# Kernel optimization log

Measured on AMD Instinct MI355X. Metric: run time of the kernel, lower is better.

## Reference

```python
import jax, jax.numpy as jnp
import numpy as np

HIDDEN = 2048
N_HEADS = 16
HEAD_DIM = HIDDEN // N_HEADS
INV_NORM = 1.0 / float(np.sqrt(HEAD_DIM))
BETA = 1.0


def setup_inputs() -> dict:
    key = jax.random.key(0)
    ks = jax.random.split(key, 12)
    B, S, H = 2, 2048, HIDDEN
    scale = 1.0 / float(np.sqrt(H))
    return {
        "hidden_states": jax.random.normal(ks[0], (B, S, H), jnp.float32),
        "residual": jax.random.normal(ks[1], (B, S, H), jnp.float32),
        "alibi": jax.random.normal(ks[2], (B * N_HEADS, 1, S), jnp.float32),
        "Wq": jax.random.normal(ks[3], (H, H), jnp.float32) * scale,
        "bq": jnp.zeros((H,), jnp.float32),
        "Wk": jax.random.normal(ks[4], (H, H), jnp.float32) * scale,
        "bk": jnp.zeros((H,), jnp.float32),
        "Wv": jax.random.normal(ks[5], (H, H), jnp.float32) * scale,
        "bv": jnp.zeros((H,), jnp.float32),
        "Wd": jax.random.normal(ks[6], (H, H), jnp.float32) * scale,
        "bd": jnp.zeros((H,), jnp.float32),
    }


def reference(hidden_states, residual, alibi, Wq, bq, Wk, bk, Wv, bv, Wd, bd):
    B, S, H = hidden_states.shape
    # separate QKV projections (nn.Linear: x @ W^T + b)
    q = hidden_states @ Wq.T + bq
    k = hidden_states @ Wk.T + bk
    v = hidden_states @ Wv.T + bv
    # [B, n_heads, S, head_dim]
    q = q.reshape(B, S, N_HEADS, HEAD_DIM).transpose(0, 2, 1, 3)
    k = k.reshape(B, S, N_HEADS, HEAD_DIM).transpose(0, 2, 1, 3)
    v = v.reshape(B, S, N_HEADS, HEAD_DIM).transpose(0, 2, 1, 3)
    # baddbmm: scores = beta * alibi + inv_norm * q @ k^T, per (batch*head)
    alibi_bh = alibi.reshape(B, N_HEADS, 1, S)  # broadcasts over query dim
    scores = BETA * alibi_bh + INV_NORM * jnp.einsum("bhqd,bhkd->bhqk", q, k)
    probs = jax.nn.softmax(scores.astype(jnp.float32), axis=-1).astype(v.dtype)
    # attention dropout: p=0.0 (identity)
    ctx = jnp.einsum("bhqk,bhkd->bhqd", probs, v)  # [B,H,S,D]
    ctx = ctx.transpose(0, 2, 1, 3).reshape(B, S, H)
    out = ctx @ Wd.T + bd
    # hidden dropout p=0.0 then residual add (dropout_add)
    return out + residual
```

## Files before the change

kernel.cpp:

```cpp
#include <hip/hip_runtime.h>

#define HID   2048
#define NHEAD 16
#define HD    128
#define SEQ   2048
#define BATCH 2
#define MROWS (BATCH*SEQ)
#define NQKV  (3*HID)
#define INV_NORM 0.08838834764831845f
#define LOG2E    1.4426950408889634f
#define SCALE_L2 (INV_NORM*LOG2E)

typedef __attribute__((ext_vector_type(8)))  __bf16 bf16x8;
typedef __attribute__((ext_vector_type(4)))  float  f32x4;
typedef __attribute__((ext_vector_type(16))) float  f32x16;

typedef __attribute__((address_space(1))) void GV;
typedef __attribute__((address_space(3))) void LV;

__device__ __forceinline__ void async16(const void* g, void* l) {
  __builtin_amdgcn_global_load_lds((const GV*)g, (LV*)l, 16, 0, 0);
}

__device__ __forceinline__ unsigned short f2bf(float f) {
  unsigned u = __builtin_bit_cast(unsigned, f);
  u += 0x7FFFu + ((u >> 16) & 1u);
  return (unsigned short)(u >> 16);
}

__device__ __forceinline__ unsigned pkbf(float a, float b) {
#if __has_builtin(__builtin_amdgcn_cvt_pk_bf16_f32)
  typedef __attribute__((ext_vector_type(2))) __bf16 bf16x2;
  bf16x2 r = __builtin_amdgcn_cvt_pk_bf16_f32(a, b);
  return __builtin_bit_cast(unsigned, r);
#else
  return (unsigned)f2bf(a) | ((unsigned)f2bf(b) << 16);
#endif
}

__device__ __forceinline__ void mfma16(f32x4& c, bf16x8 a, bf16x8 b) {
  c = __builtin_amdgcn_mfma_f32_16x16x32_bf16(a, b, c, 0, 0, 0);
}

__device__ __forceinline__ bf16x8 frag(const unsigned short* buf, int row, int chunk) {
  return *(const bf16x8*)(buf + ((row * 8 + (chunk ^ (row & 7))) << 3));
}

__global__ __launch_bounds__(256) void cvt_kernel(const float* __restrict__ src,
                                                  unsigned short* __restrict__ dst, int n) {
  int i = (blockIdx.x * 256 + threadIdx.x) * 4;
  if (i >= n) return;
  float4 v = *(const float4*)(src + i);
  ushort4 o;
  o.x = f2bf(v.x); o.y = f2bf(v.y); o.z = f2bf(v.z); o.w = f2bf(v.w);
  *(ushort4*)(dst + i) = o;
}

__global__ __launch_bounds__(256) void cvtw_kernel(const float* __restrict__ W0,
                                                   const float* __restrict__ W1,
                                                   const float* __restrict__ W2,
                                                   const float* __restrict__ W3,
                                                   unsigned short* __restrict__ dst) {
  int sel = blockIdx.y;
  const float* src = (sel == 0) ? W0 : (sel == 1) ? W1 : (sel == 2) ? W2 : W3;
  unsigned short* d = dst + (size_t)sel * HID * HID;
  int i = (blockIdx.x * 256 + threadIdx.x) * 4;
  float4 v = *(const float4*)(src + i);
  ushort4 o;
  o.x = f2bf(v.x); o.y = f2bf(v.y); o.z = f2bf(v.z); o.w = f2bf(v.w);
  *(ushort4*)(d + i) = o;
}

__device__ __forceinline__ void gemm_core(const unsigned short* __restrict__ A,
                                          const unsigned short* __restrict__ Bm,
                                          int K, int m0, int n0,
                                          unsigned short* As, unsigned short* Bs,
                                          f32x4 (&acc)[4][4]) {
  const int tid  = threadIdx.x;
  const int w    = tid >> 6;
  const int lane = tid & 63;
  const int l16  = lane & 15;
  const int quad = lane >> 4;
  const int wm   = (w & 1) * 64;
  const int wn   = (w >> 1) * 64;

  const f32x4 zero = {0.f, 0.f, 0.f, 0.f};
#pragma unroll
  for (int i = 0; i < 4; ++i)
#pragma unroll
    for (int j = 0; j < 4; ++j) acc[i][j] = zero;

  for (int k0 = 0; k0 < K; k0 += 64) {
    __syncthreads();
#pragma unroll
    for (int i = 0; i < 4; ++i) {
      int slot = i * 256 + w * 64 + lane;
      int r = slot >> 3;
      int c = (slot & 7) ^ (r & 7);
      async16(A  + (size_t)(m0 + r) * K + k0 + c * 8, (char*)As + (size_t)(i * 256 + w * 64) * 16);
      async16(Bm + (size_t)(n0 + r) * K + k0 + c * 8, (char*)Bs + (size_t)(i * 256 + w * 64) * 16);
    }
    __syncthreads();

#pragma unroll
    for (int kk = 0; kk < 2; ++kk) {
      bf16x8 af[4], bfp[4];
#pragma unroll
      for (int i = 0; i < 4; ++i) af[i]  = frag(As, wm + i * 16 + l16, kk * 4 + quad);
#pragma unroll
      for (int j = 0; j < 4; ++j) bfp[j] = frag(Bs, wn + j * 16 + l16, kk * 4 + quad);
#pragma unroll
      for (int i = 0; i < 4; ++i)
#pragma unroll
        for (int j = 0; j < 4; ++j) mfma16(acc[i][j], af[i], bfp[j]);
    }
  }
}

#define ASZ (256 * 64)

__global__ __launch_bounds__(512, 2) void gemm_qkv256_kernel(
    const unsigned short* __restrict__ Xb, const unsigned short* __restrict__ Wb,
    const float* __restrict__ bq, const float* __restrict__ bk,
    const float* __restrict__ bv, unsigned short* __restrict__ Cout) {
  __shared__ __align__(16) unsigned short As[2 * ASZ];
  __shared__ __align__(16) unsigned short Bs[2 * ASZ];

  const int tid  = threadIdx.x;
  const int w    = tid >> 6;
  const int lane = tid & 63;
  const int l16  = lane & 15;
  const int quad = lane >> 4;
  const int wm   = (w & 1) * 128;
  const int wn   = (w >> 1) * 64;

  const int wg = blockIdx.x;
  const int sw = (wg & 7) * 48 + (wg >> 3);
  const int m0 = (sw & 15) * 256;
  const int n0 = (sw >> 4) * 256;

  const unsigned short* Ag = Xb + (size_t)m0 * HID;
  const unsigned short* Bg = Wb + (size_t)n0 * HID;

  const int sr  = tid >> 3;
  const int scs = ((tid & 7) ^ (sr & 7)) * 8;

#define STG(SRC, DST, RB, KO)                                        \
  async16((SRC) + (size_t)((RB) + sr) * HID + (KO) + scs,            \
          (char*)(DST) + (((RB) * 8 + w * 64) * 16))

  f32x4 acc[8][4];
  const f32x4 zero = {0.f, 0.f, 0.f, 0.f};
#pragma unroll
  for (int a = 0; a < 8; ++a)
#pragma unroll
    for (int j = 0; j < 4; ++j) acc[a][j] = zero;

  STG(Ag, As, 0, 0);  STG(Ag, As, 64, 0);  STG(Ag, As, 128, 0);  STG(Ag, As, 192, 0);
  STG(Bg, Bs, 0, 0);  STG(Bg, Bs, 64, 0);  STG(Bg, Bs, 128, 0);  STG(Bg, Bs, 192, 0);
  STG(Ag, As + ASZ, 0, 64);  STG(Ag, As + ASZ, 128, 64);
  asm volatile("s_waitcnt vmcnt(2)" ::: "memory");
  __builtin_amdgcn_s_barrier();

  for (int i = 0; i < 16; ++i) {
    const int k1 = (2 * i + 1) * 64;
    const int t2 = 2 * i + 2, t3 = 2 * i + 3;
    const int k2 = (t2 < 32 ? t2 : 31) * 64;
    const int k3 = (t3 < 32 ? t3 : 31) * 64;
    bf16x8 tb0[4], tb1[4];

    {
      bf16x8 ta[4];
#pragma unroll
      for (int ii = 0; ii < 4; ++ii) ta[ii] = frag(As, wm + ii * 16 + l16, quad);
#pragma unroll
      for (int j = 0; j < 4; ++j) tb0[j] = frag(Bs, wn + j * 16 + l16, quad);
      STG(Ag, As + ASZ, 64, k1);
      STG(Ag, As + ASZ, 192, k1);
      __builtin_amdgcn_s_barrier();
      asm volatile("s_waitcnt lgkmcnt(0)" ::: "memory");
      __builtin_amdgcn_s_setprio(1);
#pragma unroll
      for (int ii = 0; ii < 4; ++ii)
#pragma unroll
        for (int j = 0; j < 4; ++j) mfma16(acc[ii][j], ta[ii], tb0[j]);
      __builtin_amdgcn_s_setprio(0);
      __builtin_amdgcn_s_barrier();
    }
    {
      bf16x8 ta[4];
#pragma unroll
      for (int ii = 0; ii < 4; ++ii) ta[ii] = frag(As, wm + ii * 16 + l16, 4 + quad);
#pragma unroll
      for (int j = 0; j < 4; ++j) tb1[j] = frag(Bs, wn + j * 16 + l16, 4 + quad);
      STG(Bg, Bs + ASZ, 0, k1);
      STG(Bg, Bs + ASZ, 64, k1);
      __builtin_amdgcn_s_barrier();
      asm volatile("s_waitcnt lgkmcnt(0)" ::: "memory");
      __builtin_amdgcn_s_setprio(1);
#pragma unroll
      for (int ii = 0; ii < 4; ++ii)
#pragma unroll
        for (int j = 0; j < 4; ++j) mfma16(acc[ii][j], ta[ii], tb1[j]);
      __builtin_amdgcn_s_setprio(0);
      __builtin_amdgcn_s_barrier();
    }
    {
      bf16x8 ta[4];
#pragma unroll
      for (int ii = 0; ii < 4; ++ii) ta[ii] = frag(As, wm + 64 + ii * 16 + l16, quad);
      STG(Bg, Bs + ASZ, 128, k1);
      STG(Bg, Bs + ASZ, 192, k1);
      __builtin_amdgcn_s_barrier();
      asm volatile("s_waitcnt lgkmcnt(0)" ::: "memory");
      __builtin_amdgcn_s_setprio(1);
#pragma unroll
      for (int ii = 0; ii < 4; ++ii)
#pragma unroll
        for (int j = 0; j < 4; ++j) mfma16(acc[4 + ii][j], ta[ii], tb0[j]);
      __builtin_amdgcn_s_setprio(0);
      __builtin_amdgcn_s_barrier();
    }
    {
      bf16x8 ta[4];
#pragma unroll
      for (int ii = 0; ii < 4; ++ii) ta[ii] = frag(As, wm + 64 + ii * 16 + l16, 4 + quad);
      STG(Ag, As, 0, k2);
      STG(Ag, As, 128, k2);
      __builtin_amdgcn_s_barrier();
      asm volatile("s_waitcnt lgkmcnt(0)" ::: "memory");
      __builtin_amdgcn_s_setprio(1);
#pragma unroll
      for (int ii = 0; ii < 4; ++ii)
#pragma unroll
        for (int j = 0; j < 4; ++j) mfma16(acc[4 + ii][j], ta[ii], tb1[j]);
      __builtin_amdgcn_s_setprio(0);
      asm volatile("s_waitcnt vmcnt(2)" ::: "memory");
      __builtin_amdgcn_s_barrier();
    }
    {
      bf16x8 ta[4];
#pragma unroll
      for (int ii = 0; ii < 4; ++ii) ta[ii] = frag(As + ASZ, wm + ii * 16 + l16, quad);
#pragma unroll
      for (int j = 0; j < 4; ++j) tb0[j] = frag(Bs + ASZ, wn + j * 16 + l16, quad);
      STG(Ag, As, 64, k2);
      STG(Ag, As, 192, k2);
      __builtin_amdgcn_s_barrier();
      asm volatile("s_waitcnt lgkmcnt(0)" ::: "memory");
      __builtin_amdgcn_s_setprio(1);
#pragma unroll
      for (int ii = 0; ii < 4; ++ii)
#pragma unroll
        for (int j = 0; j < 4; ++j) mfma16(acc[ii][j], ta[ii], tb0[j]);
      __builtin_amdgcn_s_setprio(0);
      __builtin_amdgcn_s_barrier();
    }
    {
      bf16x8 ta[4];
#pragma unroll
      for (int ii = 0; ii < 4; ++ii) ta[ii] = frag(As + ASZ, wm + ii * 16 + l16, 4 + quad);
#pragma unroll
      for (int j = 0; j < 4; ++j) tb1[j] = frag(Bs + ASZ, wn + j * 16 + l16, 4 + quad);
      STG(Bg, Bs, 0, k2);
      STG(Bg, Bs, 64, k2);
      __builtin_amdgcn_s_barrier();
      asm volatile("s_waitcnt lgkmcnt(0)" ::: "memory");
      __builtin_amdgcn_s_setprio(1);
#pragma unroll
      for (int ii = 0; ii < 4; ++ii)
#pragma unroll
        for (int j = 0; j < 4; ++j) mfma16(acc[ii][j], ta[ii], tb1[j]);
      __builtin_amdgcn_s_setprio(0);
      __builtin_amdgcn_s_barrier();
    }
    {
      bf16x8 ta[4];
#pragma unroll
      for (int ii = 0; ii < 4; ++ii) ta[ii] = frag(As + ASZ, wm + 64 + ii * 16 + l16, quad);
      STG(Bg, Bs, 128, k2);
      STG(Bg, Bs, 192, k2);
      __builtin_amdgcn_s_barrier();
      asm volatile("s_waitcnt lgkmcnt(0)" ::: "memory");
      __builtin_amdgcn_s_setprio(1);
#pragma unroll
      for (int ii = 0; ii < 4; ++ii)
#pragma unroll
        for (int j = 0; j < 4; ++j) mfma16(acc[4 + ii][j], ta[ii], tb0[j]);
      __builtin_amdgcn_s_setprio(0);
      __builtin_amdgcn_s_barrier();
    }
    {
      bf16x8 ta[4];
#pragma unroll
      for (int ii = 0; ii < 4; ++ii) ta[ii] = frag(As + ASZ, wm + 64 + ii * 16 + l16, 4 + quad);
      STG(Ag, As + ASZ, 0, k3);
      STG(Ag, As + ASZ, 128, k3);
      __builtin_amdgcn_s_barrier();
      asm volatile("s_waitcnt lgkmcnt(0)" ::: "memory");
      __builtin_amdgcn_s_setprio(1);
#pragma unroll
      for (int ii = 0; ii < 4; ++ii)
#pragma unroll
        for (int j = 0; j < 4; ++j) mfma16(acc[4 + ii][j], ta[ii], tb1[j]);
      __builtin_amdgcn_s_setprio(0);
      asm volatile("s_waitcnt vmcnt(2)" ::: "memory");
      __builtin_amdgcn_s_barrier();
    }
  }
#undef STG

#pragma unroll
  for (int j = 0; j < 4; ++j) {
    int ng = n0 + wn + j * 16 + l16;
    float bias = (ng < HID) ? bq[ng] : (ng < 2 * HID ? bk[ng - HID] : bv[ng - 2 * HID]);
#pragma unroll
    for (int a = 0; a < 8; ++a)
#pragma unroll
      for (int r = 0; r < 4; ++r) {
        int mg = m0 + wm + (a >> 2) * 64 + (a & 3) * 16 + quad * 4 + r;
        Cout[(size_t)mg * NQKV + ng] = f2bf(acc[a][j][r] + bias);
      }
  }
}

__global__ __launch_bounds__(256) void gemm_out_kernel(
    const unsigned short* __restrict__ Ctx, const unsigned short* __restrict__ Wdb,
    const float* __restrict__ bd, const float* __restrict__ Res,
    float* __restrict__ Out) {
  __shared__ __align__(16) unsigned short As[128 * 64];
  __shared__ __align__(16) unsigned short Bs[128 * 64];
  f32x4 acc[4][4];
  const int m0 = blockIdx.y * 128, n0 = blockIdx.x * 128;
  gemm_core(Ctx, Wdb, HID, m0, n0, As, Bs, acc);

  const int tid = threadIdx.x, w = tid >> 6, lane = tid & 63;
  const int l16 = lane & 15, quad = lane >> 4;
  const int wm = (w & 1) * 64, wn = (w >> 1) * 64;
#pragma unroll
  for (int j = 0; j < 4; ++j) {
    int ng = n0 + wn + j * 16 + l16;
    float bias = bd[ng];
#pragma unroll
    for (int i = 0; i < 4; ++i)
#pragma unroll
      for (int r = 0; r < 4; ++r) {
        int mg = m0 + wm + i * 16 + quad * 4 + r;
        size_t off = (size_t)mg * HID + ng;
        Out[off] = acc[i][j][r] + bias + Res[off];
      }
  }
}

__global__ __launch_bounds__(256) void vtrans_kernel(const unsigned short* __restrict__ QKV,
                                                     unsigned short* __restrict__ Vt) {
  __shared__ __align__(16) unsigned short T[64][72];
  const int s0 = blockIdx.x * 64, d0 = blockIdx.y * 64, bh = blockIdx.z;
  const int b = bh >> 4, h = bh & 15;
  const int tid = threadIdx.x;
#pragma unroll
  for (int i = 0; i < 2; ++i) {
    int idx = i * 256 + tid;
    int r = idx >> 3, ch = idx & 7;
    const unsigned short* g = QKV + ((size_t)b * SEQ + s0 + r) * NQKV + 2 * HID + h * HD + d0 + ch * 8;
    *(uint4*)(&T[r][ch * 8]) = *(const uint4*)g;
  }
  __syncthreads();
#pragma unroll
  for (int i = 0; i < 2; ++i) {
    int idx = i * 256 + tid;
    int d = idx >> 3, ch = idx & 7;
    unsigned short v[8];
#pragma unroll
    for (int x = 0; x < 8; ++x) v[x] = T[ch * 8 + x][d];
    unsigned short* g = Vt + ((size_t)bh * HD + d0 + d) * SEQ + s0 + ch * 8;
    *(uint4*)g = *(const uint4*)v;
  }
}

__global__ __launch_bounds__(256, 2) void attn_kernel(
    const unsigned short* __restrict__ QKV, const unsigned short* __restrict__ Vt,
    const float* __restrict__ alibi, unsigned short* __restrict__ Ctx) {
  __shared__ __align__(16) char smem[51200];
  unsigned short* Ks  = (unsigned short*)smem;
  unsigned short* Vts = (unsigned short*)(smem + 16384);
  unsigned short* Ps  = (unsigned short*)(smem + 32768);
  unsigned short* Qs  = (unsigned short*)smem;

  const int tid = threadIdx.x, w = tid >> 6, lane = tid & 63;
  const int l32 = lane & 31, h = lane >> 5;
  const int q0 = blockIdx.x * 128;
  const int bh = blockIdx.y, b = bh >> 4, hh = bh & 15;
  const size_t rowbase = (size_t)b * SEQ;
  const float* ali = alibi + (size_t)bh * SEQ;
  const unsigned short* Vbh = Vt + (size_t)bh * HD * SEQ;

  {
    const unsigned short* qbase = QKV + (rowbase + q0) * NQKV + hh * HD;
#pragma unroll
    for (int i = 0; i < 8; ++i) {
      int slot = i * 256 + w * 64 + lane;
      int r = slot >> 4, c = (slot & 15) ^ (r & 15);
      async16(qbase + (size_t)r * NQKV + c * 8, (char*)Qs + (size_t)(i * 256 + w * 64) * 16);
    }
  }
  __syncthreads();
  bf16x8 qf[8];
  {
    int qr = w * 32 + l32;
#pragma unroll
    for (int ks = 0; ks < 8; ++ks) {
      int c = (ks * 2 + h) ^ (qr & 15);
      qf[ks] = *(const bf16x8*)(Qs + (qr * 16 + c) * 8);
    }
  }

  f32x16 oacc[4];
  float l_acc = 0.f;
#pragma unroll
  for (int nb = 0; nb < 4; ++nb)
#pragma unroll
    for (int r = 0; r < 16; ++r) oacc[nb][r] = 0.f;

  __syncthreads();

  for (int kt = 0; kt < SEQ / 64; ++kt) {
    {
      const unsigned short* kbase = QKV + (rowbase + kt * 64) * NQKV + HID + hh * HD;
#pragma unroll
      for (int i = 0; i < 4; ++i) {
        int slot = i * 256 + w * 64 + lane;
        int r = slot >> 4, c = (slot & 15) ^ (r & 15);
        async16(kbase + (size_t)r * NQKV + c * 8, (char*)Ks + (size_t)(i * 256 + w * 64) * 16);
      }
      const unsigned short* vbase = Vbh + kt * 64;
#pragma unroll
      for (int i = 0; i < 4; ++i) {
        int slot = i * 256 + w * 64 + lane;
        int r = slot >> 3, c = (slot & 7) ^ (r & 7);
        async16(vbase + (size_t)r * SEQ + c * 8, (char*)Vts + (size_t)(i * 256 + w * 64) * 16);
      }
    }
    __syncthreads();

    f32x16 sacc[2];
#pragma unroll
    for (int mb = 0; mb < 2; ++mb)
#pragma unroll
      for (int r = 0; r < 16; ++r) sacc[mb][r] = 0.f;
#pragma unroll
    for (int ks = 0; ks < 8; ++ks) {
#pragma unroll
      for (int mb = 0; mb < 2; ++mb) {
        bf16x8 kf = *(const bf16x8*)(Ks + ((mb * 32 + l32) * 16 + ((ks * 2 + h) ^ (l32 & 15))) * 8);
        sacc[mb] = __builtin_amdgcn_mfma_f32_32x32x16_bf16(kf, qf[ks], sacc[mb], 0, 0, 0);
      }
    }

    const float* alik = ali + kt * 64 + 4 * h;
    const int qrow = w * 32 + l32;
#pragma unroll
    for (int mb = 0; mb < 2; ++mb) {
#pragma unroll
      for (int g = 0; g < 4; ++g) {
        float4 av = *(const float4*)(alik + mb * 32 + g * 8);
        float p0 = __builtin_amdgcn_exp2f(sacc[mb][g * 4 + 0] * SCALE_L2 + av.x * LOG2E);
        float p1 = __builtin_amdgcn_exp2f(sacc[mb][g * 4 + 1] * SCALE_L2 + av.y * LOG2E);
        float p2 = __builtin_amdgcn_exp2f(sacc[mb][g * 4 + 2] * SCALE_L2 + av.z * LOG2E);
        float p3 = __builtin_amdgcn_exp2f(sacc[mb][g * 4 + 3] * SCALE_L2 + av.w * LOG2E);
        l_acc += (p0 + p1) + (p2 + p3);
        uint2 pk;
        pk.x = pkbf(p0, p1);
        pk.y = pkbf(p2, p3);
        *(uint2*)(Ps + qrow * 72 + mb * 32 + g * 8 + 4 * h) = pk;
      }
    }

#pragma unroll
    for (int ks2 = 0; ks2 < 4; ++ks2) {
      bf16x8 pf = *(const bf16x8*)(Ps + qrow * 72 + ks2 * 16 + h * 8);
#pragma unroll
      for (int nb = 0; nb < 4; ++nb) {
        bf16x8 vf = *(const bf16x8*)(Vts + ((nb * 32 + l32) * 8 + ((ks2 * 2 + h) ^ (l32 & 7))) * 8);
        oacc[nb] = __builtin_amdgcn_mfma_f32_32x32x16_bf16(pf, vf, oacc[nb], 0, 0, 0);
      }
    }
    __syncthreads();
  }

  float lf = l_acc + __shfl_xor(l_acc, 32, 64);
  float rinv[16];
#pragma unroll
  for (int reg = 0; reg < 16; ++reg) {
    int row = (reg & 3) + 8 * (reg >> 2) + 4 * h;
    rinv[reg] = 1.0f / __shfl(lf, row, 64);
  }

#pragma unroll
  for (int nb = 0; nb < 4; ++nb)
#pragma unroll
    for (int reg = 0; reg < 16; ++reg) {
      int row = (reg & 3) + 8 * (reg >> 2) + 4 * h;
      size_t qg = rowbase + q0 + w * 32 + row;
      Ctx[qg * HID + hh * HD + nb * 32 + l32] = f2bf(oacc[nb][reg] * rinv[reg]);
    }
}

extern "C" void kernel_launch(void* const* d_in, const int* in_sizes, int n_in,
                              void* d_out, int out_size, void* d_ws, size_t ws_size,
                              hipStream_t stream) {
  const float* hidden   = (const float*)d_in[0];
  const float* residual = (const float*)d_in[1];
  const float* alibi    = (const float*)d_in[2];
  const float* Wq = (const float*)d_in[3];
  const float* bq = (const float*)d_in[4];
  const float* Wk = (const float*)d_in[5];
  const float* bk = (const float*)d_in[6];
  const float* Wv = (const float*)d_in[7];
  const float* bv = (const float*)d_in[8];
  const float* Wd = (const float*)d_in[9];
  const float* bd = (const float*)d_in[10];
  float* out = (float*)d_out;

  unsigned short* Xb    = (unsigned short*)d_ws;
  unsigned short* Wqkvb = Xb + (size_t)MROWS * HID;
  unsigned short* Wdb   = Wqkvb + (size_t)NQKV * HID;
  unsigned short* QKVb  = Wdb + (size_t)HID * HID;
  unsigned short* Ctxb  = QKVb + (size_t)MROWS * NQKV;
  unsigned short* Vtb   = Wqkvb;

  const int nX = MROWS * HID, nW = HID * HID;
  cvt_kernel<<<nX / 4 / 256, 256, 0, stream>>>(hidden, Xb, nX);
  cvtw_kernel<<<dim3(nW / 4 / 256, 4), 256, 0, stream>>>(Wq, Wk, Wv, Wd, Wqkvb);

  gemm_qkv256_kernel<<<384, 512, 0, stream>>>(Xb, Wqkvb, bq, bk, bv, QKVb);
  vtrans_kernel<<<dim3(SEQ / 64, HD / 64, BATCH * NHEAD), 256, 0, stream>>>(QKVb, Vtb);
  attn_kernel<<<dim3(SEQ / 128, BATCH * NHEAD), 256, 0, stream>>>(QKVb, Vtb, alibi, Ctxb);
  gemm_out_kernel<<<dim3(HID / 128, MROWS / 128), 256, 0, stream>>>(Ctxb, Wdb, bd, residual, out);
}
```

Before: 454.4 us.

## Deepen QKV GEMM prefetch so B tiles load a full stage ahead

```diff
diff --git a/kernel.cpp b/kernel.cpp
--- a/kernel.cpp
+++ b/kernel.cpp
@@ -156,17 +156,19 @@
 #pragma unroll
     for (int j = 0; j < 4; ++j) acc[a][j] = zero;
 
-  STG(Ag, As, 0, 0);  STG(Ag, As, 64, 0);  STG(Ag, As, 128, 0);  STG(Ag, As, 192, 0);
-  STG(Bg, Bs, 0, 0);  STG(Bg, Bs, 64, 0);  STG(Bg, Bs, 128, 0);  STG(Bg, Bs, 192, 0);
-  STG(Ag, As + ASZ, 0, 64);  STG(Ag, As + ASZ, 128, 64);
-  asm volatile("s_waitcnt vmcnt(2)" ::: "memory");
+  STG(Ag, As, 0, 0);   STG(Ag, As, 128, 0);
+  STG(Bg, Bs, 0, 0);   STG(Bg, Bs, 64, 0);  STG(Bg, Bs, 128, 0);  STG(Bg, Bs, 192, 0);
+  STG(Ag, As, 64, 0);  STG(Ag, As, 192, 0);
+  STG(Ag, As + ASZ, 0, 64);   STG(Ag, As + ASZ, 128, 64);  STG(Bg, Bs + ASZ, 0, 64);
+  STG(Bg, Bs + ASZ, 64, 64);  STG(Bg, Bs + ASZ, 128, 64);  STG(Bg, Bs + ASZ, 192, 64);
+  asm volatile("s_waitcnt vmcnt(8)" ::: "memory");
   __builtin_amdgcn_s_barrier();
 
   for (int i = 0; i < 16; ++i) {
-    const int k1 = (2 * i + 1) * 64;
-    const int t2 = 2 * i + 2, t3 = 2 * i + 3;
-    const int k2 = (t2 < 32 ? t2 : 31) * 64;
-    const int k3 = (t3 < 32 ? t3 : 31) * 64;
+    const int ko  = (2 * i + 1) * 64;
+    const int t2  = 2 * i + 2, t3 = 2 * i + 3;
+    const int ke  = (t2 < 32 ? t2 : 31) * 64;
+    const int ko2 = (t3 < 32 ? t3 : 31) * 64;
     bf16x8 tb0[4], tb1[4];
 
     {
@@ -175,8 +177,8 @@
       for (int ii = 0; ii < 4; ++ii) ta[ii] = frag(As, wm + ii * 16 + l16, quad);
 #pragma unroll
       for (int j = 0; j < 4; ++j) tb0[j] = frag(Bs, wn + j * 16 + l16, quad);
-      STG(Ag, As + ASZ, 64, k1);
-      STG(Ag, As + ASZ, 192, k1);
+      STG(Ag, As + ASZ, 64, ko);
+      STG(Ag, As + ASZ, 192, ko);
       __builtin_amdgcn_s_barrier();
       asm volatile("s_waitcnt lgkmcnt(0)" ::: "memory");
       __builtin_amdgcn_s_setprio(1);
@@ -193,8 +195,6 @@
       for (int ii = 0; ii < 4; ++ii) ta[ii] = frag(As, wm + ii * 16 + l16, 4 + quad);
 #pragma unroll
       for (int j = 0; j < 4; ++j) tb1[j] = frag(Bs, wn + j * 16 + l16, 4 + quad);
-      STG(Bg, Bs + ASZ, 0, k1);
-      STG(Bg, Bs + ASZ, 64, k1);
       __builtin_amdgcn_s_barrier();
       asm volatile("s_waitcnt lgkmcnt(0)" ::: "memory");
       __builtin_amdgcn_s_setprio(1);
@@ -203,14 +203,16 @@
 #pragma unroll
         for (int j = 0; j < 4; ++j) mfma16(acc[ii][j], ta[ii], tb1[j]);
       __builtin_amdgcn_s_setprio(0);
+      asm volatile("s_waitcnt vmcnt(8)" ::: "memory");
       __builtin_amdgcn_s_barrier();
     }
     {
       bf16x8 ta[4];
 #pragma unroll
       for (int ii = 0; ii < 4; ++ii) ta[ii] = frag(As, wm + 64 + ii * 16 + l16, quad);
-      STG(Bg, Bs + ASZ, 128, k1);
-      STG(Bg, Bs + ASZ, 192, k1);
+      STG(Ag, As, 0, ke);
+      STG(Ag, As, 128, ke);
+      STG(Bg, Bs, 0, ke);
       __builtin_amdgcn_s_barrier();
       asm volatile("s_waitcnt lgkmcnt(0)" ::: "memory");
       __builtin_amdgcn_s_setprio(1);
@@ -225,8 +227,9 @@
       bf16x8 ta[4];
 #pragma unroll
       for (int ii = 0; ii < 4; ++ii) ta[ii] = frag(As, wm + 64 + ii * 16 + l16, 4 + quad);
-      STG(Ag, As, 0, k2);
-      STG(Ag, As, 128, k2);
+      STG(Bg, Bs, 64, ke);
+      STG(Bg, Bs, 128, ke);
+      STG(Bg, Bs, 192, ke);
       __builtin_amdgcn_s_barrier();
       asm volatile("s_waitcnt lgkmcnt(0)" ::: "memory");
       __builtin_amdgcn_s_setprio(1);
@@ -235,7 +238,7 @@
 #pragma unroll
         for (int j = 0; j < 4; ++j) mfma16(acc[4 + ii][j], ta[ii], tb1[j]);
       __builtin_amdgcn_s_setprio(0);
-      asm volatile("s_waitcnt vmcnt(2)" ::: "memory");
+      asm volatile("s_waitcnt vmcnt(8)" ::: "memory");
       __builtin_amdgcn_s_barrier();
     }
     {
@@ -244,8 +247,8 @@
       for (int ii = 0; ii < 4; ++ii) ta[ii] = frag(As + ASZ, wm + ii * 16 + l16, quad);
 #pragma unroll
       for (int j = 0; j < 4; ++j) tb0[j] = frag(Bs + ASZ, wn + j * 16 + l16, quad);
-      STG(Ag, As, 64, k2);
-      STG(Ag, As, 192, k2);
+      STG(Ag, As, 64, ke);
+      STG(Ag, As, 192, ke);
       __builtin_amdgcn_s_barrier();
       asm volatile("s_waitcnt lgkmcnt(0)" ::: "memory");
       __builtin_amdgcn_s_setprio(1);
@@ -262,8 +265,6 @@
       for (int ii = 0; ii < 4; ++ii) ta[ii] = frag(As + ASZ, wm + ii * 16 + l16, 4 + quad);
 #pragma unroll
       for (int j = 0; j < 4; ++j) tb1[j] = frag(Bs + ASZ, wn + j * 16 + l16, 4 + quad);
-      STG(Bg, Bs, 0, k2);
-      STG(Bg, Bs, 64, k2);
       __builtin_amdgcn_s_barrier();
       asm volatile("s_waitcnt lgkmcnt(0)" ::: "memory");
       __builtin_amdgcn_s_setprio(1);
@@ -272,14 +273,16 @@
 #pragma unroll
         for (int j = 0; j < 4; ++j) mfma16(acc[ii][j], ta[ii], tb1[j]);
       __builtin_amdgcn_s_setprio(0);
+      asm volatile("s_waitcnt vmcnt(8)" ::: "memory");
       __builtin_amdgcn_s_barrier();
     }
     {
       bf16x8 ta[4];
 #pragma unroll
       for (int ii = 0; ii < 4; ++ii) ta[ii] = frag(As + ASZ, wm + 64 + ii * 16 + l16, quad);
-      STG(Bg, Bs, 128, k2);
-      STG(Bg, Bs, 192, k2);
+      STG(Ag, As + ASZ, 0, ko2);
+      STG(Ag, As + ASZ, 128, ko2);
+      STG(Bg, Bs + ASZ, 0, ko2);
       __builtin_amdgcn_s_barrier();
       asm volatile("s_waitcnt lgkmcnt(0)" ::: "memory");
       __builtin_amdgcn_s_setprio(1);
@@ -294,8 +297,9 @@
       bf16x8 ta[4];
 #pragma unroll
       for (int ii = 0; ii < 4; ++ii) ta[ii] = frag(As + ASZ, wm + 64 + ii * 16 + l16, 4 + quad);
-      STG(Ag, As + ASZ, 0, k3);
-      STG(Ag, As + ASZ, 128, k3);
+      STG(Bg, Bs + ASZ, 64, ko2);
+      STG(Bg, Bs + ASZ, 128, ko2);
+      STG(Bg, Bs + ASZ, 192, ko2);
       __builtin_amdgcn_s_barrier();
       asm volatile("s_waitcnt lgkmcnt(0)" ::: "memory");
       __builtin_amdgcn_s_setprio(1);
@@ -304,7 +308,7 @@
 #pragma unroll
         for (int j = 0; j < 4; ++j) mfma16(acc[4 + ii][j], ta[ii], tb1[j]);
       __builtin_amdgcn_s_setprio(0);
-      asm volatile("s_waitcnt vmcnt(2)" ::: "memory");
+      asm volatile("s_waitcnt vmcnt(8)" ::: "memory");
       __builtin_amdgcn_s_barrier();
     }
   }
```

Result: slower. 476.0 us (+4.7%).
